# Performance work log

Hardware: AMD Instinct MI355X
Metric: run time of the kernel (lower is better)

## Reference

```python
import jax, jax.numpy as jnp
import numpy as np

TRANSLATE_STD = 0.125
SCALE_STD = 0.2
CUTOUT_SIZE = 0.5

B, C, H, W = 64, 3, 512, 512


def setup_inputs() -> dict:
    key = jax.random.key(0)
    ks = jax.random.split(key, 20)
    inp = {
        'images': jax.random.normal(ks[0], (B, C, H, W), dtype=jnp.float32),
        'u_angle': jax.random.uniform(ks[1], (B,), dtype=jnp.float32),
        'u_scale': jax.random.uniform(ks[2], (B,), dtype=jnp.float32),
        'u_trans': jax.random.uniform(ks[3], (B,), dtype=jnp.float32),
        'u_bright': jax.random.uniform(ks[4], (B,), dtype=jnp.float32),
        'u_contrast': jax.random.uniform(ks[5], (B,), dtype=jnp.float32),
        'u_sat': jax.random.uniform(ks[6], (B,), dtype=jnp.float32),
        'noise': jax.random.normal(ks[7], (B, C, H, W), dtype=jnp.float32),
        'm_flip': jax.random.randint(ks[8], (B,), 0, 2, dtype=jnp.int32),
        'm_rot': jax.random.randint(ks[9], (B,), 0, 2, dtype=jnp.int32),
        'm_scale': jax.random.randint(ks[10], (B,), 0, 2, dtype=jnp.int32),
        'm_trans': jax.random.randint(ks[11], (B,), 0, 2, dtype=jnp.int32),
        'm_bright': jax.random.randint(ks[12], (B,), 0, 2, dtype=jnp.int32),
        'm_contrast': jax.random.randint(ks[13], (B,), 0, 2, dtype=jnp.int32),
        'm_sat': jax.random.randint(ks[14], (B,), 0, 2, dtype=jnp.int32),
        'm_cut': jax.random.randint(ks[15], (B,), 0, 2, dtype=jnp.int32),
        'y0': jax.random.randint(ks[16], (B,), 0, H - int(H * CUTOUT_SIZE) + 1, dtype=jnp.int32),
        'x0': jax.random.randint(ks[17], (B,), 0, W - int(W * CUTOUT_SIZE) + 1, dtype=jnp.int32),
    }
    return inp


def _sample_bilinear_reflect(img, gx, gy):
    # img: [C,H,W]; gx, gy: [H,W] normalized coords in grid_sample convention
    # (align_corners=False, padding_mode='reflection')
    c, h, w = img.shape
    x = ((gx + 1.0) * w - 1.0) * 0.5
    y = ((gy + 1.0) * h - 1.0) * 0.5

    def reflect(v, size):
        # reflect about pixel edges [-0.5, size-0.5], then clip coordinate
        v = jnp.abs(v + 0.5)
        v = jnp.mod(v, 2.0 * size)
        v = jnp.minimum(v, 2.0 * size - v)
        return jnp.clip(v - 0.5, 0.0, size - 1.0)

    x = reflect(x, float(w))
    y = reflect(y, float(h))
    x0f = jnp.floor(x)
    y0f = jnp.floor(y)
    wx = x - x0f
    wy = y - y0f
    x0i = jnp.clip(x0f, 0, w - 1).astype(jnp.int32)
    x1i = jnp.clip(x0f + 1, 0, w - 1).astype(jnp.int32)
    y0i = jnp.clip(y0f, 0, h - 1).astype(jnp.int32)
    y1i = jnp.clip(y0f + 1, 0, h - 1).astype(jnp.int32)
    v00 = img[:, y0i, x0i]
    v01 = img[:, y0i, x1i]
    v10 = img[:, y1i, x0i]
    v11 = img[:, y1i, x1i]
    top = v00 + wx * (v01 - v00)
    bot = v10 + wx * (v11 - v10)
    return top + wy * (bot - top)


def reference(images, u_angle, u_scale, u_trans, u_bright, u_contrast, u_sat,
              noise, m_flip, m_rot, m_scale, m_trans, m_bright, m_contrast,
              m_sat, m_cut, y0, x0):
    b, c, h, w = images.shape
    # xflip
    images = jnp.where((m_flip > 0)[:, None, None, None], images[..., ::-1], images)
    # rotate / scale / translate (single value broadcast to both axes, as in original)
    angle = jnp.where(m_rot > 0, (u_angle * 2.0 - 1.0) * jnp.pi, 0.0)
    sc = jnp.where(m_scale > 0, (u_scale * 2.0 - 1.0) * SCALE_STD + 1.0, 1.0)
    tr = jnp.where(m_trans > 0, (u_trans * 2.0 - 1.0) * TRANSLATE_STD, 0.0)
    ca = jnp.cos(angle)[:, None, None]
    sa = jnp.sin(angle)[:, None, None]
    scb = sc[:, None, None]
    trb = tr[:, None, None]
    gx0, gy0 = jnp.meshgrid(jnp.linspace(-1.0, 1.0, w), jnp.linspace(-1.0, 1.0, h), indexing='xy')  # [H,W]
    gx = scb * (ca * gx0 - sa * gy0) + trb  # [B,H,W]
    gy = scb * (sa * gx0 + ca * gy0) + trb
    images = jax.vmap(_sample_bilinear_reflect)(images, gx, gy)
    # brightness
    bb = jnp.where(m_bright > 0, u_bright * 0.2, 0.0)
    images = jnp.clip(images + bb[:, None, None, None], -1.0, 1.0)
    # contrast
    cc = jnp.where(m_contrast > 0, u_contrast + 0.5, 1.0)
    images = jnp.clip(images * cc[:, None, None, None], -1.0, 1.0)
    # saturation: lerp(grayscale, images, s)
    ss = jnp.where(m_sat > 0, u_sat * 2.0, 1.0)[:, None, None, None]
    gray = images.mean(axis=1, keepdims=True)
    images = jnp.clip(gray + ss * (images - gray), -1.0, 1.0)
    ch, cw = int(h * CUTOUT_SIZE), int(w * CUTOUT_SIZE)
    ys = jnp.arange(h)[None, :, None]
    xs = jnp.arange(w)[None, None, :]
    y0b = y0[:, None, None]
    x0b = x0[:, None, None]
    cmask = (ys >= y0b) & (ys < y0b + ch) & (xs >= x0b) & (xs < x0b + cw)
    fmask = cmask & (m_cut > 0)[:, None, None]
    images = jnp.where(fmask[:, None, :, :], noise, images)
    return images
```

## Files before the change

kernel.cpp:

```cpp
#include <hip/hip_runtime.h>
#include <math.h>


constexpr int Bn = 64;
constexpr int Cn = 3;
constexpr int Hn = 512;
constexpr int Wn = 512;
constexpr float TRANSLATE_STD = 0.125f;
constexpr float SCALE_STD = 0.2f;
constexpr int CUT_H = 256;
constexpr int CUT_W = 256;

constexpr int LDS_CAP = 1280;

typedef float f2v __attribute__((ext_vector_type(2)));

__device__ __forceinline__ f2v load2(const float* p) {
    f2v r;
    __builtin_memcpy(&r, p, 8);
    return r;
}

__device__ __forceinline__ float reflect_coord(float v, float size) {
    v = fabsf(v + 0.5f);
    v = fmodf(v, 2.0f * size);
    v = fminf(v, 2.0f * size - v);
    return fminf(fmaxf(v - 0.5f, 0.0f), size - 1.0f);
}

__global__ __launch_bounds__(256) void augment_kernel(
    const float* __restrict__ images,
    const float* __restrict__ u_angle,
    const float* __restrict__ u_scale,
    const float* __restrict__ u_trans,
    const float* __restrict__ u_bright,
    const float* __restrict__ u_contrast,
    const float* __restrict__ u_sat,
    const float* __restrict__ noise,
    const int* __restrict__ m_flip,
    const int* __restrict__ m_rot,
    const int* __restrict__ m_scale,
    const int* __restrict__ m_trans,
    const int* __restrict__ m_bright,
    const int* __restrict__ m_contrast,
    const int* __restrict__ m_sat,
    const int* __restrict__ m_cut,
    const int* __restrict__ y0p,
    const int* __restrict__ x0p,
    float* __restrict__ out)
{
    __shared__ float lds[Cn * LDS_CAP];

    const int x = blockIdx.x * 32 + threadIdx.x;
    const int y = blockIdx.y * 8 + threadIdx.y;
    const int b = blockIdx.z;

    const float angle = (m_rot[b] > 0) ? (u_angle[b] * 2.0f - 1.0f) * 3.14159265358979323846f : 0.0f;
    const float sc    = (m_scale[b] > 0) ? (u_scale[b] * 2.0f - 1.0f) * SCALE_STD + 1.0f : 1.0f;
    const float tr    = (m_trans[b] > 0) ? (u_trans[b] * 2.0f - 1.0f) * TRANSLATE_STD : 0.0f;
    const float bb    = (m_bright[b] > 0) ? u_bright[b] * 0.2f : 0.0f;
    const float cc    = (m_contrast[b] > 0) ? u_contrast[b] + 0.5f : 1.0f;
    const float ss    = (m_sat[b] > 0) ? u_sat[b] * 2.0f : 1.0f;
    const bool  flip  = m_flip[b] > 0;
    const bool  docut = m_cut[b] > 0;
    const int   cy0   = y0p[b];
    const int   cx0   = x0p[b];

    float saf, caf;
    __sincosf(angle, &saf, &caf);

    auto coord = [&](float fx, float fy, float& oxx, float& oyy) {
        const float gx0 = -1.0f + (2.0f / 511.0f) * fx;
        const float gy0 = -1.0f + (2.0f / 511.0f) * fy;
        const float gx = sc * (caf * gx0 - saf * gy0) + tr;
        const float gy = sc * (saf * gx0 + caf * gy0) + tr;
        oxx = ((gx + 1.0f) * (float)Wn - 1.0f) * 0.5f;
        oyy = ((gy + 1.0f) * (float)Hn - 1.0f) * 0.5f;
    };

    float xx, yy;
    coord((float)x, (float)y, xx, yy);

    const float tx0 = (float)(blockIdx.x * 32);
    const float tx1 = tx0 + 31.0f;
    const float ty0 = (float)(blockIdx.y * 8);
    const float ty1 = ty0 + 7.0f;
    float cxx0, cyy0, cxx1, cyy1, cxx2, cyy2, cxx3, cyy3;
    coord(tx0, ty0, cxx0, cyy0);
    coord(tx1, ty0, cxx1, cyy1);
    coord(tx0, ty1, cxx2, cyy2);
    coord(tx1, ty1, cxx3, cyy3);
    const float minxx = fminf(fminf(cxx0, cxx1), fminf(cxx2, cxx3));
    const float maxxx = fmaxf(fmaxf(cxx0, cxx1), fmaxf(cxx2, cxx3));
    const float minyy = fminf(fminf(cyy0, cyy1), fminf(cyy2, cyy3));
    const float maxyy = fmaxf(fmaxf(cyy0, cyy1), fmaxf(cyy2, cyy3));

    bool staged = (minxx >= -0.9f) && (maxxx <= 511.9f) &&
                  (minyy >= -0.9f) && (maxyy <= 511.9f);

    int x_lo = 0, x_hi = 1, y_lo = 0, y_hi = 1, fw = 2, fh = 2;
    if (staged) {
        x_lo = max(0, (int)floorf(minxx));
        x_hi = min(Wn - 1, (int)floorf(maxxx) + 1);
        x_lo = max(0, min(x_lo, x_hi - 1));
        y_lo = max(0, (int)floorf(minyy));
        y_hi = min(Hn - 1, (int)floorf(maxyy) + 1);
        y_lo = max(0, min(y_lo, y_hi - 1));
        fw = x_hi - x_lo + 1;
        fh = y_hi - y_lo + 1;
        if (fw * fh > LDS_CAP) staged = false;
    }

    const size_t plane = (size_t)Hn * Wn;
    const float* imgb = images + (size_t)b * Cn * plane;

    float vals[Cn];

    if (staged) {
        #pragma unroll
        for (int c = 0; c < Cn; ++c) {
            const float* src = imgb + (size_t)c * plane;
            float* dst = &lds[c * LDS_CAP];
            for (int ry = threadIdx.y; ry < fh; ry += 8) {
                const float* rowp = src + (size_t)(y_lo + ry) * Wn;
                for (int rx = threadIdx.x; rx < fw; rx += 32) {
                    const int gxc = x_lo + rx;
                    dst[ry * fw + rx] = rowp[flip ? (Wn - 1 - gxc) : gxc];
                }
            }
        }
        __syncthreads();

        const float x0f = floorf(xx);
        const float y0f = floorf(yy);
        const float wx = xx - x0f;
        const float wy = yy - y0f;
        const int x0i = (int)x0f;
        const int y0i = (int)y0f;

        const int xa = min(max(x0i, x_lo), x_hi);
        const int xb = min(max(x0i + 1, x_lo), x_hi);
        const int pb = min(xa, x_hi - 1);
        const bool s0 = (xa != pb);
        const bool s1 = (xb != pb);
        const int ya = min(max(y0i, y_lo), y_hi) - y_lo;
        const int yb = min(max(y0i + 1, y_lo), y_hi) - y_lo;
        const int col = pb - x_lo;
        const int off0 = ya * fw + col;
        const int off1 = yb * fw + col;

        #pragma unroll
        for (int c = 0; c < Cn; ++c) {
            const float* ch = &lds[c * LDS_CAP];
            const float t0x = ch[off0], t0y = ch[off0 + 1];
            const float t1x = ch[off1], t1y = ch[off1 + 1];
            const float v00 = s0 ? t0y : t0x;
            const float v01 = s1 ? t0y : t0x;
            const float v10 = s0 ? t1y : t1x;
            const float v11 = s1 ? t1y : t1x;
            const float top = v00 + wx * (v01 - v00);
            const float bot = v10 + wx * (v11 - v10);
            float v = top + wy * (bot - top);
            v = fminf(fmaxf(v + bb, -1.0f), 1.0f);
            v = fminf(fmaxf(v * cc, -1.0f), 1.0f);
            vals[c] = v;
        }
    } else {
        const float rxx = reflect_coord(xx, (float)Wn);
        const float ryy = reflect_coord(yy, (float)Hn);

        const float x0f = floorf(rxx);
        const float y0f = floorf(ryy);
        const float wx = rxx - x0f;
        const float wy = ryy - y0f;

        int x0i = (int)fminf(fmaxf(x0f, 0.0f), (float)(Wn - 1));
        int x1i = (int)fminf(x0f + 1.0f, (float)(Wn - 1));
        const int y0i = (int)fminf(fmaxf(y0f, 0.0f), (float)(Hn - 1));
        const int y1i = (int)fminf(y0f + 1.0f, (float)(Hn - 1));

        if (flip) { x0i = (Wn - 1) - x0i; x1i = (Wn - 1) - x1i; }

        const int xbase = min(min(x0i, x1i), Wn - 2);
        const bool s0 = (x0i != xbase);
        const bool s1 = (x1i != xbase);

        const int r0 = y0i * Wn + xbase;
        const int r1 = y1i * Wn + xbase;

        #pragma unroll
        for (int c = 0; c < Cn; ++c) {
            const float* p = imgb + (size_t)c * plane;
            const f2v t0 = load2(p + r0);
            const f2v t1 = load2(p + r1);
            const float v00 = s0 ? t0.y : t0.x;
            const float v01 = s1 ? t0.y : t0.x;
            const float v10 = s0 ? t1.y : t1.x;
            const float v11 = s1 ? t1.y : t1.x;
            const float top = v00 + wx * (v01 - v00);
            const float bot = v10 + wx * (v11 - v10);
            float v = top + wy * (bot - top);
            v = fminf(fmaxf(v + bb, -1.0f), 1.0f);
            v = fminf(fmaxf(v * cc, -1.0f), 1.0f);
            vals[c] = v;
        }
    }

    const float gray = (vals[0] + vals[1] + vals[2]) * (1.0f / 3.0f);
    const bool cut = docut && (y >= cy0) && (y < cy0 + CUT_H) && (x >= cx0) && (x < cx0 + CUT_W);

    const size_t base = (size_t)b * Cn * plane + (size_t)y * Wn + (size_t)x;
    #pragma unroll
    for (int c = 0; c < Cn; ++c) {
        float v = gray + ss * (vals[c] - gray);
        v = fminf(fmaxf(v, -1.0f), 1.0f);
        if (cut) v = __builtin_nontemporal_load(&noise[base + c * plane]);
        __builtin_nontemporal_store(v, &out[base + c * plane]);
    }
}

extern "C" void kernel_launch(void* const* d_in, const int* in_sizes, int n_in,
                              void* d_out, int out_size, void* d_ws, size_t ws_size,
                              hipStream_t stream) {
    const float* images     = (const float*)d_in[0];
    const float* u_angle    = (const float*)d_in[1];
    const float* u_scale    = (const float*)d_in[2];
    const float* u_trans    = (const float*)d_in[3];
    const float* u_bright   = (const float*)d_in[4];
    const float* u_contrast = (const float*)d_in[5];
    const float* u_sat      = (const float*)d_in[6];
    const float* noise      = (const float*)d_in[7];
    const int*   m_flip     = (const int*)d_in[8];
    const int*   m_rot      = (const int*)d_in[9];
    const int*   m_scale    = (const int*)d_in[10];
    const int*   m_trans    = (const int*)d_in[11];
    const int*   m_bright   = (const int*)d_in[12];
    const int*   m_contrast = (const int*)d_in[13];
    const int*   m_sat      = (const int*)d_in[14];
    const int*   m_cut      = (const int*)d_in[15];
    const int*   y0p        = (const int*)d_in[16];
    const int*   x0p        = (const int*)d_in[17];
    float* out = (float*)d_out;

    dim3 block(32, 8);
    dim3 grid(Wn / 32, Hn / 8, Bn);
    augment_kernel<<<grid, block, 0, stream>>>(
        images, u_angle, u_scale, u_trans, u_bright, u_contrast, u_sat, noise,
        m_flip, m_rot, m_scale, m_trans, m_bright, m_contrast, m_sat, m_cut,
        y0p, x0p, out);
}
```

Before: 634.0 us.

## Use square 16x16 tiles with fixed 32-wide padded LDS footprint

Changes the output tile from 32x8 to 16x16 so that a rotated tile's source footprint is smaller. The LDS staging buffer becomes a fixed 32-column window with stride 34 and up to 32 rows, and each thread copies one column with a simple strided row loop instead of a nested variable-width loop. Tiles whose footprint is wider than 32 columns or taller than 32 rows (large scale or rotation) fall back to the global-memory path. This shrinks redundant halo loads and makes the staging loop cheaper, at the cost of more fallback blocks and extra rows loaded per tile.

```diff
diff --git a/kernel.cpp b/kernel.cpp
--- a/kernel.cpp
+++ b/kernel.cpp
@@ -11,7 +11,10 @@
 constexpr int CUT_H = 256;
 constexpr int CUT_W = 256;
 
-constexpr int LDS_CAP = 1280;
+constexpr int FW = 32;
+constexpr int FSTRIDE = 34;
+constexpr int FH_MAX = 32;
+constexpr int CH_LDS = FSTRIDE * FH_MAX;
 
 typedef float f2v __attribute__((ext_vector_type(2)));
 
@@ -49,10 +52,10 @@
     const int* __restrict__ x0p,
     float* __restrict__ out)
 {
-    __shared__ float lds[Cn * LDS_CAP];
-
-    const int x = blockIdx.x * 32 + threadIdx.x;
-    const int y = blockIdx.y * 8 + threadIdx.y;
+    __shared__ float lds[Cn * CH_LDS];
+
+    const int x = blockIdx.x * 16 + threadIdx.x;
+    const int y = blockIdx.y * 16 + threadIdx.y;
     const int b = blockIdx.z;
 
     const float angle = (m_rot[b] > 0) ? (u_angle[b] * 2.0f - 1.0f) * 3.14159265358979323846f : 0.0f;
@@ -81,10 +84,10 @@
     float xx, yy;
     coord((float)x, (float)y, xx, yy);
 
-    const float tx0 = (float)(blockIdx.x * 32);
-    const float tx1 = tx0 + 31.0f;
-    const float ty0 = (float)(blockIdx.y * 8);
-    const float ty1 = ty0 + 7.0f;
+    const float tx0 = (float)(blockIdx.x * 16);
+    const float tx1 = tx0 + 15.0f;
+    const float ty0 = (float)(blockIdx.y * 16);
+    const float ty1 = ty0 + 15.0f;
     float cxx0, cyy0, cxx1, cyy1, cxx2, cyy2, cxx3, cyy3;
     coord(tx0, ty0, cxx0, cyy0);
     coord(tx1, ty0, cxx1, cyy1);
@@ -98,17 +101,14 @@
     bool staged = (minxx >= -0.9f) && (maxxx <= 511.9f) &&
                   (minyy >= -0.9f) && (maxyy <= 511.9f);
 
-    int x_lo = 0, x_hi = 1, y_lo = 0, y_hi = 1, fw = 2, fh = 2;
+    int x_lo = 0, x_hi = 1, y_lo = 0, y_hi = 1, fh = 1;
     if (staged) {
-        x_lo = max(0, (int)floorf(minxx));
-        x_hi = min(Wn - 1, (int)floorf(maxxx) + 1);
-        x_lo = max(0, min(x_lo, x_hi - 1));
-        y_lo = max(0, (int)floorf(minyy));
-        y_hi = min(Hn - 1, (int)floorf(maxyy) + 1);
-        y_lo = max(0, min(y_lo, y_hi - 1));
-        fw = x_hi - x_lo + 1;
+        x_lo = min(max((int)floorf(minxx) - 1, 0), Wn - FW);
+        x_hi = x_lo + FW - 1;
+        y_lo = max((int)floorf(minyy) - 1, 0);
+        y_hi = min((int)floorf(maxyy) + 2, Hn - 1);
         fh = y_hi - y_lo + 1;
-        if (fw * fh > LDS_CAP) staged = false;
+        if (fh > FH_MAX || ((int)floorf(maxxx) + 1) > x_hi) staged = false;
     }
 
     const size_t plane = (size_t)Hn * Wn;
@@ -117,16 +117,16 @@
     float vals[Cn];
 
     if (staged) {
+        const int tid = threadIdx.y * 16 + threadIdx.x;
+        const int srx = tid & 31;
+        const int sry = tid >> 5;
+        const int gcol = flip ? (Wn - 1 - (x_lo + srx)) : (x_lo + srx);
         #pragma unroll
         for (int c = 0; c < Cn; ++c) {
-            const float* src = imgb + (size_t)c * plane;
-            float* dst = &lds[c * LDS_CAP];
-            for (int ry = threadIdx.y; ry < fh; ry += 8) {
-                const float* rowp = src + (size_t)(y_lo + ry) * Wn;
-                for (int rx = threadIdx.x; rx < fw; rx += 32) {
-                    const int gxc = x_lo + rx;
-                    dst[ry * fw + rx] = rowp[flip ? (Wn - 1 - gxc) : gxc];
-                }
+            const float* srcc = imgb + (size_t)c * plane + gcol;
+            float* dstc = &lds[c * CH_LDS];
+            for (int r = sry; r < fh; r += 8) {
+                dstc[r * FSTRIDE + srx] = srcc[(size_t)(y_lo + r) * Wn];
             }
         }
         __syncthreads();
@@ -146,12 +146,12 @@
         const int ya = min(max(y0i, y_lo), y_hi) - y_lo;
         const int yb = min(max(y0i + 1, y_lo), y_hi) - y_lo;
         const int col = pb - x_lo;
-        const int off0 = ya * fw + col;
-        const int off1 = yb * fw + col;
+        const int off0 = ya * FSTRIDE + col;
+        const int off1 = yb * FSTRIDE + col;
 
         #pragma unroll
         for (int c = 0; c < Cn; ++c) {
-            const float* ch = &lds[c * LDS_CAP];
+            const float* ch = &lds[c * CH_LDS];
             const float t0x = ch[off0], t0y = ch[off0 + 1];
             const float t1x = ch[off1], t1y = ch[off1 + 1];
             const float v00 = s0 ? t0y : t0x;
@@ -242,8 +242,8 @@
     const int*   x0p        = (const int*)d_in[17];
     float* out = (float*)d_out;
 
-    dim3 block(32, 8);
-    dim3 grid(Wn / 32, Hn / 8, Bn);
+    dim3 block(16, 16);
+    dim3 grid(Wn / 16, Hn / 16, Bn);
     augment_kernel<<<grid, block, 0, stream>>>(
         images, u_angle, u_scale, u_trans, u_bright, u_contrast, u_sat, noise,
         m_flip, m_rot, m_scale, m_trans, m_bright, m_contrast, m_sat, m_cut,
```

Result: faster. 589.5 us (-7.0%).
